# Optimization experiments

Hardware: AMD Instinct MI355X
Metric: run time of the kernel (lower is better)

The kernel has to match this reference:

```python
import jax, jax.numpy as jnp
import numpy as np

NSEQ, T, OBS, ACT, H = 256, 1024, 128, 16, 64


def setup_inputs() -> dict:
    key = jax.random.key(0)
    ks = jax.random.split(key, 16)
    N = NSEQ * T
    obs = jax.random.normal(ks[0], (N, OBS), jnp.float32)
    action = jax.random.randint(ks[1], (N,), 0, ACT)
    ep = (jax.random.uniform(ks[2], (NSEQ, T)) < 0.02).astype(jnp.float32)
    ep = ep.at[:, 0].set(1.0)  # every padded sequence starts an episode
    episode_starts = ep.reshape(-1)
    z = lambda *s: jnp.zeros(s, jnp.float32)
    W = lambda k, shape, s=0.1: jax.random.normal(k, shape, jnp.float32) * s
    d = dict(
        obs=obs, action=action, episode_starts=episode_starts,
        h_pi=z(1, NSEQ, H), c_pi=z(1, NSEQ, H), h_vf=z(1, NSEQ, H), c_vf=z(1, NSEQ, H),
        Wp1=W(ks[3], (64, OBS)), bp1=z(64), Wp2=W(ks[4], (64, 64)), bp2=z(64),
        Wv1=W(ks[5], (64, OBS)), bv1=z(64), Wv2=W(ks[6], (64, 64)), bv2=z(64),
        Wih_pi=W(ks[7], (4 * H, 64)), Whh_pi=W(ks[8], (4 * H, H)), bih_pi=z(4 * H), bhh_pi=z(4 * H),
        Wih_vf=W(ks[9], (4 * H, 64)), Whh_vf=W(ks[10], (4 * H, H)), bih_vf=z(4 * H), bhh_vf=z(4 * H),
        Wa=W(ks[11], (ACT, H), 0.01), ba=z(ACT), Wc=W(ks[12], (1, H), 1.0), bc=z(1),
    )
    return d


def _mlp(x, W1, b1, W2, b2):
    # shared Linear->Tanh->Linear->Tanh feature extractor
    return jnp.tanh(jnp.tanh(x @ W1.T + b1) @ W2.T + b2)


def _lstm(feats, ep, h0, c0, Wih, Whh, bih, bhh):
    # feats: (NSEQ*T, 64) flattened as (n_seq, T); scan over time with episode-reset masking
    xs = feats.reshape(NSEQ, T, -1).transpose(1, 0, 2)  # (T, n_seq, 64)
    eps = ep.reshape(NSEQ, T).T                          # (T, n_seq)
    b = bih + bhh

    def step(carry, inp):
        h, c = carry
        x, e = inp
        m = (1.0 - e)[:, None]
        h = h * m
        c = c * m
        g = x @ Wih.T + h @ Whh.T + b                    # (n_seq, 4H), gate order i,f,g,o
        i, f, gg, o = jnp.split(g, 4, axis=-1)
        c = jax.nn.sigmoid(f) * c + jax.nn.sigmoid(i) * jnp.tanh(gg)
        h = jax.nn.sigmoid(o) * jnp.tanh(c)
        return (h, c), h

    _, outs = jax.lax.scan(step, (h0[0], c0[0]), (xs, eps))
    return outs.transpose(1, 0, 2).reshape(-1, H)        # (NSEQ*T, H)


def reference(obs, action, episode_starts, h_pi, c_pi, h_vf, c_vf,
              Wp1, bp1, Wp2, bp2, Wv1, bv1, Wv2, bv2,
              Wih_pi, Whh_pi, bih_pi, bhh_pi, Wih_vf, Whh_vf, bih_vf, bhh_vf,
              Wa, ba, Wc, bc):
    feat_pi = _mlp(obs, Wp1, bp1, Wp2, bp2)
    feat_vf = _mlp(obs, Wv1, bv1, Wv2, bv2)
    lat_pi = _lstm(feat_pi, episode_starts, h_pi, c_pi, Wih_pi, Whh_pi, bih_pi, bhh_pi)
    lat_vf = _lstm(feat_vf, episode_starts, h_vf, c_vf, Wih_vf, Whh_vf, bih_vf, bhh_vf)
    logits = lat_pi @ Wa.T + ba
    logp = jax.nn.log_softmax(logits, axis=-1)
    logprob = jnp.take_along_axis(logp, action[:, None], axis=-1)[:, 0]
    entropy = -jnp.sum(jnp.exp(logp) * logp, axis=-1)
    value = lat_vf @ Wc.T + bc
    return logprob, entropy, value
```

## Files before the change

### kernel.cpp

```cpp
#include <hip/hip_runtime.h>


#define NSEQ  256
#define TT    1024
#define NROWS (NSEQ * TT)
#define OBS   128
#define ACTN  16
#define HH    64
#define MAXEP NROWS

__device__ __forceinline__ float frcp(float x)  { return __builtin_amdgcn_rcpf(x); }
__device__ __forceinline__ float fsigm(float x) { return frcp(1.f + __expf(-x)); }
__device__ __forceinline__ float ftanh(float x) { return 1.f - 2.f * frcp(1.f + __expf(2.f * x)); }

__global__ void lstm_ac_zero(int* ctrs, int* hist) {
    const int t = threadIdx.x;
    hist[t] = 0;
    if (t < 8) ctrs[t] = 0;
}

__global__ void lstm_ac_episodes(const float* __restrict__ ep,
                                 int* __restrict__ ctrs, int* __restrict__ hist,
                                 int2* __restrict__ raw) {
    __shared__ float flags[TT];
    const int s = blockIdx.x;
    for (int i = threadIdx.x; i < TT; i += blockDim.x) flags[i] = ep[(size_t)s * TT + i];
    __syncthreads();
    for (int t0 = threadIdx.x; t0 < TT; t0 += blockDim.x) {
        const bool start = (t0 == 0) || (flags[t0] > 0.5f);
        if (start) {
            int t1 = t0 + 1;
            while (t1 < TT && !(flags[t1] > 0.5f)) t1++;
            const int len = t1 - t0;
            const int slot = atomicAdd(&ctrs[0], 1);
            raw[slot] = make_int2(s * TT + t0, len);
            atomicAdd(&hist[len - 1], 1);
        }
    }
}

__global__ void lstm_ac_prefix(const int* __restrict__ hist, int* __restrict__ offs) {
    __shared__ int a[1024];
    const int tid = threadIdx.x;
    const int h0 = hist[tid];
    a[tid] = h0;
    __syncthreads();
    for (int s = 1; s < 1024; s <<= 1) {
        const int v = (tid + s < 1024) ? a[tid + s] : 0;
        __syncthreads();
        a[tid] += v;
        __syncthreads();
    }
    offs[tid] = a[tid] - h0;
}

__global__ void lstm_ac_scatter(const int* __restrict__ ctrs, const int2* __restrict__ raw,
                                int* __restrict__ offs, int2* __restrict__ sorted) {
    const int i = blockIdx.x * 256 + threadIdx.x;
    if (i < ctrs[0]) {
        const int2 e = raw[i];
        const int slot = atomicAdd(&offs[e.y - 1], 1);
        sorted[slot] = e;
    }
}

__global__ __launch_bounds__(256, 2) void lstm_ac_feat(
    const float* __restrict__ obs,
    const float* __restrict__ W1, const float* __restrict__ b1,
    const float* __restrict__ W2, const float* __restrict__ b2,
    float* __restrict__ feat) {
    __shared__ float x_lds[4][OBS];
    __shared__ float l1_lds[4][HH];
    const int tid = threadIdx.x;
    const int w = tid >> 6, j = tid & 63;

    float w1r[OBS], w2r[HH];
    {
        const float4* p1 = (const float4*)(W1 + (size_t)j * OBS);
#pragma unroll
        for (int q = 0; q < OBS / 4; q++) {
            float4 v = p1[q];
            w1r[4*q] = v.x; w1r[4*q+1] = v.y; w1r[4*q+2] = v.z; w1r[4*q+3] = v.w;
        }
        const float4* p2 = (const float4*)(W2 + (size_t)j * HH);
#pragma unroll
        for (int q = 0; q < HH / 4; q++) {
            float4 v = p2[q];
            w2r[4*q] = v.x; w2r[4*q+1] = v.y; w2r[4*q+2] = v.z; w2r[4*q+3] = v.w;
        }
    }
    const float bb1 = b1[j], bb2 = b2[j];
    const int gw = blockIdx.x * 4 + w;

    for (int rr = 0; rr < 32; ++rr) {
        const int r = gw * 32 + rr;
        x_lds[w][j]      = obs[(size_t)r * OBS + j];
        x_lds[w][HH + j] = obs[(size_t)r * OBS + HH + j];
        const float4* xv4 = (const float4*)x_lds[w];
        float sa[4] = {0.f, 0.f, 0.f, 0.f};
#pragma unroll
        for (int q = 0; q < OBS / 4; q++) {
            float4 v = xv4[q];
            sa[q & 3] += v.x * w1r[4*q] + v.y * w1r[4*q+1] + v.z * w1r[4*q+2] + v.w * w1r[4*q+3];
        }
        const float l1 = ftanh(bb1 + (sa[0] + sa[1]) + (sa[2] + sa[3]));
        l1_lds[w][j] = l1;
        const float4* lv4 = (const float4*)l1_lds[w];
        float ta[4] = {0.f, 0.f, 0.f, 0.f};
#pragma unroll
        for (int q = 0; q < HH / 4; q++) {
            float4 v = lv4[q];
            ta[q & 3] += v.x * w2r[4*q] + v.y * w2r[4*q+1] + v.z * w2r[4*q+2] + v.w * w2r[4*q+3];
        }
        feat[(size_t)r * HH + j] = ftanh(bb2 + (ta[0] + ta[1]) + (ta[2] + ta[3]));
    }
}

__global__ __launch_bounds__(512, 3) void lstm_ac_scan(
    float* __restrict__ fl_pi, float* __restrict__ fl_vf,
    const float* __restrict__ Wih_pi, const float* __restrict__ Whh_pi,
    const float* __restrict__ bih_pi, const float* __restrict__ bhh_pi,
    const float* __restrict__ Wih_vf, const float* __restrict__ Whh_vf,
    const float* __restrict__ bih_vf, const float* __restrict__ bhh_vf,
    int* __restrict__ ctrs, const int2* __restrict__ sorted) {
    __shared__ float x_lds[4][HH];
    __shared__ float h_lds[4][HH];
    __shared__ float g_lds[4][4 * HH];
    __shared__ int task_s;

    const int tid = threadIdx.x;
    const int w   = tid >> 6;
    const int l   = tid & 63;
    const int g   = (w << 5) + (l >> 1);
    const int kh  = l & 1;
    const int kbase = kh * 32;
    const bool upd = (w < 4);
    const int b_me = upd ? w : (w - 4);
    const int j = l;
    const bool is_tanh_gate = ((w >> 1) == 2);

    const int cnt = ctrs[0];
    const int G = (cnt + 3) >> 2;
    const int ntasks = 2 * G;

    int cur = -1;
    float wih[32], whh[32];
    float bg = 0.f;
    float* fl = fl_pi;
    float c_reg = 0.f;

    for (;;) {
        __syncthreads();
        if (tid == 0) task_s = atomicAdd(&ctrs[1], 1);
        __syncthreads();
        const int task = task_s;
        if (task >= ntasks) break;
        const int lstm = (task >= G) ? 1 : 0;
        const int gq = lstm ? (task - G) : task;
        if (lstm != cur) {
            cur = lstm;
            const float* Wih = lstm ? Wih_vf : Wih_pi;
            const float* Whh = lstm ? Whh_vf : Whh_pi;
            const float* bih = lstm ? bih_vf : bih_pi;
            const float* bhh = lstm ? bhh_vf : bhh_pi;
            fl = lstm ? fl_vf : fl_pi;
            const float4* p1 = (const float4*)(Wih + (size_t)g * HH + kbase);
            const float4* p2 = (const float4*)(Whh + (size_t)g * HH + kbase);
#pragma unroll
            for (int q = 0; q < 8; q++) {
                float4 a = p1[q];
                wih[4*q+0] = a.x; wih[4*q+1] = a.y; wih[4*q+2] = a.z; wih[4*q+3] = a.w;
                float4 b = p2[q];
                whh[4*q+0] = b.x; whh[4*q+1] = b.y; whh[4*q+2] = b.z; whh[4*q+3] = b.w;
            }
            bg = (kh == 0) ? (bih[g] + bhh[g]) : 0.f;
        }

        int r0[4], ln[4];
#pragma unroll
        for (int s = 0; s < 4; s++) {
            const int idx = gq * 4 + s;
            if (idx < cnt) { const int2 e = sorted[idx]; r0[s] = e.x; ln[s] = e.y; }
            else { r0[s] = 0; ln[s] = 0; }
        }
        const int maxlen = ln[0];

        if (upd) { h_lds[b_me][j] = 0.f; c_reg = 0.f; }
        else if (ln[b_me] > 0) x_lds[b_me][j] = fl[(size_t)r0[b_me] * HH + j];
        __syncthreads();

        for (int t = 0; t < maxlen; ++t) {
            float xnext = 0.f;
            if (!upd) {
                const int tn = t + 1;
                const int rr = (tn < ln[b_me]) ? (r0[b_me] + tn) : r0[b_me];
                xnext = fl[(size_t)rr * HH + j];
            }
#pragma unroll
            for (int b = 0; b < 4; b++) {
                if (t < ln[b]) {
                    const float4* xv = (const float4*)&x_lds[b][kbase];
                    const float4* hv = (const float4*)&h_lds[b][kbase];
                    float a0 = bg, a1 = 0.f, a2 = 0.f, a3 = 0.f;
#pragma unroll
                    for (int q = 0; q < 8; q++) {
                        const float4 x4 = xv[q];
                        const float4 h4 = hv[q];
                        a0 += x4.x * wih[4*q+0] + h4.x * whh[4*q+0];
                        a1 += x4.y * wih[4*q+1] + h4.y * whh[4*q+1];
                        a2 += x4.z * wih[4*q+2] + h4.z * whh[4*q+2];
                        a3 += x4.w * wih[4*q+3] + h4.w * whh[4*q+3];
                    }
                    float part = (a0 + a1) + (a2 + a3);
                    part += __shfl_xor(part, 1, 64);
                    g_lds[b][g] = is_tanh_gate ? ftanh(part) : fsigm(part);
                }
            }
            __syncthreads();
            if (upd) {
                if (t < ln[b_me]) {
                    const float gi = g_lds[b_me][j];
                    const float gf = g_lds[b_me][HH + j];
                    const float gg = g_lds[b_me][2 * HH + j];
                    const float go = g_lds[b_me][3 * HH + j];
                    c_reg = gf * c_reg + gi * gg;
                    const float h = go * ftanh(c_reg);
                    h_lds[b_me][j] = h;
                    fl[(size_t)(r0[b_me] + t) * HH + j] = h;
                }
            } else {
                if (t + 1 < ln[b_me]) x_lds[b_me][j] = xnext;
            }
            __syncthreads();
        }
    }
}

__global__ __launch_bounds__(256) void lstm_ac_heads(
    const float* __restrict__ lat_pi, const float* __restrict__ lat_vf,
    const int* __restrict__ action,
    const float* __restrict__ Wa, const float* __restrict__ ba,
    const float* __restrict__ Wc, const float* __restrict__ bc,
    float* __restrict__ out) {
    const int r = blockIdx.x * 256 + threadIdx.x;
    float4 lp[16];
    const float4* pp = (const float4*)(lat_pi + (size_t)r * HH);
#pragma unroll
    for (int q = 0; q < 16; q++) lp[q] = pp[q];

    float logits[ACTN];
#pragma unroll
    for (int a = 0; a < ACTN; a++) {
        const float4* wp = (const float4*)(Wa + (size_t)a * HH);
        float s0 = 0.f, s1 = 0.f, s2 = 0.f, s3 = 0.f;
#pragma unroll
        for (int q = 0; q < 16; q++) {
            const float4 wv = wp[q];
            s0 += lp[q].x * wv.x; s1 += lp[q].y * wv.y;
            s2 += lp[q].z * wv.z; s3 += lp[q].w * wv.w;
        }
        logits[a] = ba[a] + (s0 + s1) + (s2 + s3);
    }
    float m = logits[0];
#pragma unroll
    for (int a = 1; a < ACTN; a++) m = fmaxf(m, logits[a]);
    float s0 = 0.f, s1 = 0.f;
#pragma unroll
    for (int a = 0; a < ACTN; a++) {
        const float e = __expf(logits[a] - m);
        s0 += e;
        s1 += e * logits[a];
    }
    const float lse = m + __logf(s0);
    const int act = action[r];
    float la = logits[0];
#pragma unroll
    for (int a = 1; a < ACTN; a++) la = (act == a) ? logits[a] : la;
    out[r] = la - lse;
    out[NROWS + r] = lse - s1 * frcp(s0);

    const float4* pv = (const float4*)(lat_vf + (size_t)r * HH);
    const float4* wc4 = (const float4*)Wc;
    float t0 = 0.f, t1 = 0.f, t2 = 0.f, t3 = 0.f;
#pragma unroll
    for (int q = 0; q < 16; q++) {
        const float4 v = pv[q];
        const float4 wv = wc4[q];
        t0 += v.x * wv.x; t1 += v.y * wv.y; t2 += v.z * wv.z; t3 += v.w * wv.w;
    }
    out[2 * (size_t)NROWS + r] = bc[0] + (t0 + t1) + (t2 + t3);
}

extern "C" void kernel_launch(void* const* d_in, const int* in_sizes, int n_in,
                              void* d_out, int out_size, void* d_ws, size_t ws_size,
                              hipStream_t stream) {
    const float* obs    = (const float*)d_in[0];
    const int*   action = (const int*)d_in[1];
    const float* epst   = (const float*)d_in[2];
    const float* Wp1 = (const float*)d_in[7];
    const float* bp1 = (const float*)d_in[8];
    const float* Wp2 = (const float*)d_in[9];
    const float* bp2 = (const float*)d_in[10];
    const float* Wv1 = (const float*)d_in[11];
    const float* bv1 = (const float*)d_in[12];
    const float* Wv2 = (const float*)d_in[13];
    const float* bv2 = (const float*)d_in[14];
    const float* Wih_pi = (const float*)d_in[15];
    const float* Whh_pi = (const float*)d_in[16];
    const float* bih_pi = (const float*)d_in[17];
    const float* bhh_pi = (const float*)d_in[18];
    const float* Wih_vf = (const float*)d_in[19];
    const float* Whh_vf = (const float*)d_in[20];
    const float* bih_vf = (const float*)d_in[21];
    const float* bhh_vf = (const float*)d_in[22];
    const float* Wa = (const float*)d_in[23];
    const float* ba = (const float*)d_in[24];
    const float* Wc = (const float*)d_in[25];
    const float* bc = (const float*)d_in[26];
    float* out = (float*)d_out;

    char* ws = (char*)d_ws;
    int*  ctrs   = (int*)ws;
    int*  hist   = (int*)(ws + 32);
    int*  offs   = (int*)(ws + 32 + 4096);
    int2* raw    = (int2*)(ws + 32 + 8192);
    int2* sorted = raw + MAXEP;
    float* fl_pi = (float*)((char*)(sorted + MAXEP));
    float* fl_vf = fl_pi + (size_t)NROWS * HH;

    lstm_ac_zero<<<1, 1024, 0, stream>>>(ctrs, hist);
    lstm_ac_episodes<<<NSEQ, 256, 0, stream>>>(epst, ctrs, hist, raw);
    lstm_ac_feat<<<2048, 256, 0, stream>>>(obs, Wp1, bp1, Wp2, bp2, fl_pi);
    lstm_ac_feat<<<2048, 256, 0, stream>>>(obs, Wv1, bv1, Wv2, bv2, fl_vf);
    lstm_ac_prefix<<<1, 1024, 0, stream>>>(hist, offs);
    lstm_ac_scatter<<<1024, 256, 0, stream>>>(ctrs, raw, offs, sorted);
    lstm_ac_scan<<<1024, 512, 0, stream>>>(fl_pi, fl_vf,
                                           Wih_pi, Whh_pi, bih_pi, bhh_pi,
                                           Wih_vf, Whh_vf, bih_vf, bhh_vf,
                                           ctrs, sorted);
    lstm_ac_heads<<<NROWS / 256, 256, 0, stream>>>(fl_pi, fl_vf, action,
                                                   Wa, ba, Wc, bc, out);
}
```

Baseline: 1.907 ms.

## Merge feature launches, prefetch obs rows, pin waves-per-EU, scalarize scan episode arrays

The two feature-extractor launches are merged into one grid of 4096 blocks, where the block index selects the policy or value weights. The obs row for the next iteration is now loaded into registers before the current row is processed. The scan kernel's per-group r0/ln arrays are replaced by scalar variables and a macro-unrolled gate loop, so the arrays are not placed in scratch memory. amdgpu_waves_per_eu attributes are added to the feat, scan and heads kernels to control register allocation and occupancy, which may raise register pressure or cause spills.

```diff
diff --git a/kernel.cpp b/kernel.cpp
--- a/kernel.cpp
+++ b/kernel.cpp
@@ -64,15 +64,24 @@
     }
 }
 
-__global__ __launch_bounds__(256, 2) void lstm_ac_feat(
+__global__ __launch_bounds__(256) __attribute__((amdgpu_waves_per_eu(2, 2)))
+void lstm_ac_feat(
     const float* __restrict__ obs,
-    const float* __restrict__ W1, const float* __restrict__ b1,
-    const float* __restrict__ W2, const float* __restrict__ b2,
-    float* __restrict__ feat) {
+    const float* __restrict__ Wp1, const float* __restrict__ bp1,
+    const float* __restrict__ Wp2, const float* __restrict__ bp2,
+    const float* __restrict__ Wv1, const float* __restrict__ bv1,
+    const float* __restrict__ Wv2, const float* __restrict__ bv2,
+    float* __restrict__ fl_pi, float* __restrict__ fl_vf) {
     __shared__ float x_lds[4][OBS];
     __shared__ float l1_lds[4][HH];
     const int tid = threadIdx.x;
     const int w = tid >> 6, j = tid & 63;
+    const int half = blockIdx.x >> 11;
+    const float* W1 = half ? Wv1 : Wp1;
+    const float* b1 = half ? bv1 : bp1;
+    const float* W2 = half ? Wv2 : Wp2;
+    const float* b2 = half ? bv2 : bp2;
+    float* feat = half ? fl_vf : fl_pi;
 
     float w1r[OBS], w2r[HH];
     {
@@ -90,12 +99,18 @@
         }
     }
     const float bb1 = b1[j], bb2 = b2[j];
-    const int gw = blockIdx.x * 4 + w;
-
+    const int gw = (blockIdx.x & 2047) * 4 + w;
+
+    float xa = obs[(size_t)(gw * 32) * OBS + j];
+    float xb = obs[(size_t)(gw * 32) * OBS + HH + j];
     for (int rr = 0; rr < 32; ++rr) {
         const int r = gw * 32 + rr;
-        x_lds[w][j]      = obs[(size_t)r * OBS + j];
-        x_lds[w][HH + j] = obs[(size_t)r * OBS + HH + j];
+        x_lds[w][j]      = xa;
+        x_lds[w][HH + j] = xb;
+        if (rr + 1 < 32) {
+            xa = obs[(size_t)(r + 1) * OBS + j];
+            xb = obs[(size_t)(r + 1) * OBS + HH + j];
+        }
         const float4* xv4 = (const float4*)x_lds[w];
         float sa[4] = {0.f, 0.f, 0.f, 0.f};
 #pragma unroll
@@ -116,7 +131,8 @@
     }
 }
 
-__global__ __launch_bounds__(512, 3) void lstm_ac_scan(
+__global__ __launch_bounds__(512) __attribute__((amdgpu_waves_per_eu(4, 4)))
+void lstm_ac_scan(
     float* __restrict__ fl_pi, float* __restrict__ fl_vf,
     const float* __restrict__ Wih_pi, const float* __restrict__ Whh_pi,
     const float* __restrict__ bih_pi, const float* __restrict__ bhh_pi,
@@ -176,49 +192,53 @@
             bg = (kh == 0) ? (bih[g] + bhh[g]) : 0.f;
         }
 
-        int r0[4], ln[4];
-#pragma unroll
-        for (int s = 0; s < 4; s++) {
-            const int idx = gq * 4 + s;
-            if (idx < cnt) { const int2 e = sorted[idx]; r0[s] = e.x; ln[s] = e.y; }
-            else { r0[s] = 0; ln[s] = 0; }
-        }
-        const int maxlen = ln[0];
+        const int base = gq * 4;
+        int2 e;
+        e = (base + 0 < cnt) ? sorted[base + 0] : make_int2(0, 0); const int r00 = e.x, ln0 = e.y;
+        e = (base + 1 < cnt) ? sorted[base + 1] : make_int2(0, 0); const int r01 = e.x, ln1 = e.y;
+        e = (base + 2 < cnt) ? sorted[base + 2] : make_int2(0, 0); const int r02 = e.x, ln2 = e.y;
+        e = (base + 3 < cnt) ? sorted[base + 3] : make_int2(0, 0); const int r03 = e.x, ln3 = e.y;
+        const int r0_me = (b_me == 0) ? r00 : (b_me == 1) ? r01 : (b_me == 2) ? r02 : r03;
+        const int ln_me = (b_me == 0) ? ln0 : (b_me == 1) ? ln1 : (b_me == 2) ? ln2 : ln3;
+        const int maxlen = ln0;
 
         if (upd) { h_lds[b_me][j] = 0.f; c_reg = 0.f; }
-        else if (ln[b_me] > 0) x_lds[b_me][j] = fl[(size_t)r0[b_me] * HH + j];
+        else if (ln_me > 0) x_lds[b_me][j] = fl[(size_t)r0_me * HH + j];
         __syncthreads();
 
         for (int t = 0; t < maxlen; ++t) {
             float xnext = 0.f;
             if (!upd) {
                 const int tn = t + 1;
-                const int rr = (tn < ln[b_me]) ? (r0[b_me] + tn) : r0[b_me];
+                const int rr = (tn < ln_me) ? (r0_me + tn) : r0_me;
                 xnext = fl[(size_t)rr * HH + j];
             }
-#pragma unroll
-            for (int b = 0; b < 4; b++) {
-                if (t < ln[b]) {
-                    const float4* xv = (const float4*)&x_lds[b][kbase];
-                    const float4* hv = (const float4*)&h_lds[b][kbase];
-                    float a0 = bg, a1 = 0.f, a2 = 0.f, a3 = 0.f;
-#pragma unroll
-                    for (int q = 0; q < 8; q++) {
-                        const float4 x4 = xv[q];
-                        const float4 h4 = hv[q];
-                        a0 += x4.x * wih[4*q+0] + h4.x * whh[4*q+0];
-                        a1 += x4.y * wih[4*q+1] + h4.y * whh[4*q+1];
-                        a2 += x4.z * wih[4*q+2] + h4.z * whh[4*q+2];
-                        a3 += x4.w * wih[4*q+3] + h4.w * whh[4*q+3];
-                    }
-                    float part = (a0 + a1) + (a2 + a3);
-                    part += __shfl_xor(part, 1, 64);
-                    g_lds[b][g] = is_tanh_gate ? ftanh(part) : fsigm(part);
-                }
+#define GATE_B(B, LNB)                                                          \
+            if (t < LNB) {                                                      \
+                const float4* xv = (const float4*)&x_lds[B][kbase];             \
+                const float4* hv = (const float4*)&h_lds[B][kbase];             \
+                float a0 = bg, a1 = 0.f, a2 = 0.f, a3 = 0.f;                    \
+                _Pragma("unroll")                                               \
+                for (int q = 0; q < 8; q++) {                                   \
+                    const float4 x4 = xv[q];                                    \
+                    const float4 h4 = hv[q];                                    \
+                    a0 += x4.x * wih[4*q+0] + h4.x * whh[4*q+0];                \
+                    a1 += x4.y * wih[4*q+1] + h4.y * whh[4*q+1];                \
+                    a2 += x4.z * wih[4*q+2] + h4.z * whh[4*q+2];                \
+                    a3 += x4.w * wih[4*q+3] + h4.w * whh[4*q+3];                \
+                }                                                               \
+                float part = (a0 + a1) + (a2 + a3);                             \
+                part += __shfl_xor(part, 1, 64);                                \
+                g_lds[B][g] = is_tanh_gate ? ftanh(part) : fsigm(part);         \
             }
+            GATE_B(0, ln0)
+            GATE_B(1, ln1)
+            GATE_B(2, ln2)
+            GATE_B(3, ln3)
+#undef GATE_B
             __syncthreads();
             if (upd) {
-                if (t < ln[b_me]) {
+                if (t < ln_me) {
                     const float gi = g_lds[b_me][j];
                     const float gf = g_lds[b_me][HH + j];
                     const float gg = g_lds[b_me][2 * HH + j];
@@ -226,17 +246,18 @@
                     c_reg = gf * c_reg + gi * gg;
                     const float h = go * ftanh(c_reg);
                     h_lds[b_me][j] = h;
-                    fl[(size_t)(r0[b_me] + t) * HH + j] = h;
+                    fl[(size_t)(r0_me + t) * HH + j] = h;
                 }
             } else {
-                if (t + 1 < ln[b_me]) x_lds[b_me][j] = xnext;
+                if (t + 1 < ln_me) x_lds[b_me][j] = xnext;
             }
             __syncthreads();
         }
     }
 }
 
-__global__ __launch_bounds__(256) void lstm_ac_heads(
+__global__ __launch_bounds__(256) __attribute__((amdgpu_waves_per_eu(4, 4)))
+void lstm_ac_heads(
     const float* __restrict__ lat_pi, const float* __restrict__ lat_vf,
     const int* __restrict__ action,
     const float* __restrict__ Wa, const float* __restrict__ ba,
@@ -330,8 +351,8 @@
 
     lstm_ac_zero<<<1, 1024, 0, stream>>>(ctrs, hist);
     lstm_ac_episodes<<<NSEQ, 256, 0, stream>>>(epst, ctrs, hist, raw);
-    lstm_ac_feat<<<2048, 256, 0, stream>>>(obs, Wp1, bp1, Wp2, bp2, fl_pi);
-    lstm_ac_feat<<<2048, 256, 0, stream>>>(obs, Wv1, bv1, Wv2, bv2, fl_vf);
+    lstm_ac_feat<<<4096, 256, 0, stream>>>(obs, Wp1, bp1, Wp2, bp2,
+                                           Wv1, bv1, Wv2, bv2, fl_pi, fl_vf);
     lstm_ac_prefix<<<1, 1024, 0, stream>>>(hist, offs);
     lstm_ac_scatter<<<1024, 256, 0, stream>>>(ctrs, raw, offs, sorted);
     lstm_ac_scan<<<1024, 512, 0, stream>>>(fl_pi, fl_vf,
```

Measured after the change: 1.797 ms. 1.06x faster.
